# Kernel tuning notes

Hardware: AMD Instinct MI355X
Metric: run time of the kernel (lower is better)

Reference implementation:

```python
import jax, jax.numpy as jnp
import numpy as np

B, C, H, W = 8, 2048, 14, 14
NUM_CLASSES, WORD_DIM, INTER_DIM = 80, 300, 1024


def setup_inputs() -> dict:
    key = jax.random.key(0)
    ks = jax.random.split(key, 8)
    s = 0.02
    return {
        "image_features": jax.random.normal(ks[0], (B, C, H, W), jnp.float32),
        "word_features": jax.random.normal(ks[1], (NUM_CLASSES, WORD_DIM), jnp.float32),
        "W1": jax.random.normal(ks[2], (INTER_DIM, C), jnp.float32) * s,
        "W2": jax.random.normal(ks[3], (INTER_DIM, WORD_DIM), jnp.float32) * s,
        "W3": jax.random.normal(ks[4], (INTER_DIM, INTER_DIM), jnp.float32) * s,
        "b3": jax.random.normal(ks[5], (INTER_DIM,), jnp.float32) * s,
        "Wa": jax.random.normal(ks[6], (1, INTER_DIM), jnp.float32) * s,
        "ba": jax.random.normal(ks[7], (1,), jnp.float32) * s,
        "num_classes": NUM_CLASSES,
    }


def reference(image_features, word_features, W1, W2, W3, b3, Wa, ba, num_classes):
    b, c, h, w = image_features.shape
    # [s, b, c] with s = h*w (spatial locations)
    img = image_features.reshape(b, c, h * w).transpose(2, 0, 1)
    f_wh = img @ W1.T                      # [s, b, D]
    f_wd = word_features @ W2.T            # [n, D]
    # additive-attention score MLP; broadcast to [s, b, n, D]
    lb = jnp.tanh(f_wh[:, :, None, :] * f_wd[None, None, :, :]) @ W3.T + b3
    coef = (lb @ Wa.T + ba)[..., 0]        # [s, b, n]
    coef = jax.nn.softmax(coef, axis=0)    # softmax over spatial locations
    # weighted sum over spatial dim -> [b, n, c]
    return jnp.einsum('sbc,sbn->bnc', img, coef)
```

## Files before the change

kernel.cpp:

```cpp
#include <hip/hip_runtime.h>
#include <math.h>

#define SB 196
#define SP 224
#define NB 8
#define NC 2048
#define ND 1024
#define NN 80
#define NW 300
#define CH 8
#define DCH (ND / CH)

typedef __bf16 v8bf __attribute__((ext_vector_type(8)));
typedef __bf16 v4bf __attribute__((ext_vector_type(4)));
typedef __bf16 v2bf __attribute__((ext_vector_type(2)));
typedef float  f32x4 __attribute__((ext_vector_type(4)));

__global__ __launch_bounds__(256) void k0_v(const float* __restrict__ W3,
                                            const float* __restrict__ Wa,
                                            float* __restrict__ v) {
    int d  = blockIdx.x * 256 + threadIdx.x;
    int e0 = blockIdx.y * 64;
    float p = 0.f;
    #pragma unroll 8
    for (int e = e0; e < e0 + 64; ++e) {
        p += Wa[e] * W3[(size_t)e * ND + d];
    }
    atomicAdd(&v[d], p);
}

__global__ __launch_bounds__(256) void k0_fwd(const float* __restrict__ word,
                                              const float* __restrict__ W2,
                                              const float* __restrict__ v,
                                              float2* __restrict__ wpack) {
    __shared__ __align__(16) float lword[NW];
    int n = blockIdx.x;
    int d = blockIdx.y * 256 + threadIdx.x;
    for (int i = threadIdx.x; i < NW; i += 256) lword[i] = word[(size_t)n * NW + i];
    __syncthreads();
    const float4* wr = (const float4*)(W2 + (size_t)d * NW);
    const float4* l4 = (const float4*)lword;
    float acc = 0.f;
    #pragma unroll 5
    for (int i = 0; i < NW / 4; ++i) {
        float4 a = wr[i], b = l4[i];
        acc += a.x * b.x + a.y * b.y + a.z * b.z + a.w * b.w;
    }
    float2 o;
    o.x = 2.8853900817779268f * acc;
    o.y = -2.f * v[d];
    wpack[(size_t)n * ND + d] = o;
}

__global__ __launch_bounds__(256) void kcast_x(const float* __restrict__ X,
                                               const float* __restrict__ W1,
                                               __bf16* __restrict__ Xt,
                                               __bf16* __restrict__ Xhi,
                                               __bf16* __restrict__ Xlo,
                                               __bf16* __restrict__ W1b) {
    const int t = threadIdx.x;
    if (blockIdx.z == 8) {
        unsigned int slice_tid = (blockIdx.x * 4 + blockIdx.y) * 256 + t;
        #pragma unroll 4
        for (int r = 0; r < 16; ++r) {
            size_t i = ((size_t)slice_tid + (size_t)r * 32768) * 4;
            float4 f = *(const float4*)(W1 + i);
            v4bf o;
            o[0] = (__bf16)f.x; o[1] = (__bf16)f.y;
            o[2] = (__bf16)f.z; o[3] = (__bf16)f.w;
            *(v4bf*)(W1b + i) = o;
        }
        return;
    }
    __shared__ float tile[64][65];
    const int b  = blockIdx.z;
    const int c0 = blockIdx.x * 64;
    const int s0 = blockIdx.y * 64;
    const float* Xb = X + (size_t)b * NC * SB;
    {
        int ss = t & 63, cbase = t >> 6;
        #pragma unroll
        for (int r = 0; r < 16; ++r) {
            int cc = cbase + 4 * r;
            float val = (s0 + ss < SB) ? Xb[(size_t)(c0 + cc) * SB + s0 + ss] : 0.f;
            tile[cc][ss] = val;
        }
    }
    __syncthreads();
    {
        int cc = t & 63, sbase = t >> 6;
        #pragma unroll
        for (int r = 0; r < 16; ++r) {
            int ss = sbase + 4 * r;
            if (s0 + ss < SB)
                Xt[((size_t)b * SB + s0 + ss) * NC + c0 + cc] = (__bf16)tile[cc][ss];
        }
    }
    {
        int ss = t & 63, cbase = t >> 6;
        int sg = s0 + ss;
        #pragma unroll
        for (int r = 0; r < 16; ++r) {
            int cc = cbase + 4 * r;
            if (sg < SP) {
                float val = (sg < SB) ? tile[cc][ss] : 0.f;
                __bf16 h = (__bf16)val;
                __bf16 l = (__bf16)(val - (float)h);
                size_t base = ((size_t)b * NC + c0 + cc) * SP + sg;
                Xhi[base] = h;
                Xlo[base] = l;
            }
        }
    }
}

#define PITCH 40
__global__ __launch_bounds__(256) void k1_mfma(const __bf16* __restrict__ Xt,
                                               const __bf16* __restrict__ W1b,
                                               float* __restrict__ F) {
    __shared__ __align__(16) __bf16 lA[64 * PITCH];
    __shared__ __align__(16) __bf16 lB[64 * PITCH];
    const int t    = threadIdx.x;
    const int d0   = blockIdx.x * 64;
    const int s0   = blockIdx.y * 64;
    const int b    = blockIdx.z;
    const int lane = t & 63;
    const int wave = t >> 6;
    const int doff = (wave & 1) * 32;
    const int soff = (wave >> 1) * 32;
    const int quad = lane >> 4;
    const int l16  = lane & 15;

    f32x4 acc[2][2] = {};

    const int rr = t >> 2;
    const int cc = (t & 3) * 8;
    const bool sv = (s0 + rr) < SB;
    const __bf16* Ag = W1b + (size_t)(d0 + rr) * NC + cc;
    const __bf16* Bg = Xt + ((size_t)b * SB + (sv ? (s0 + rr) : 0)) * NC + cc;
    __bf16* lAw = lA + rr * PITCH + cc;
    __bf16* lBw = lB + rr * PITCH + cc;

    const __bf16* rA0 = lA + (doff + l16) * PITCH + quad * 8;
    const __bf16* rA1 = rA0 + 16 * PITCH;
    const __bf16* rB0 = lB + (soff + l16) * PITCH + quad * 8;
    const __bf16* rB1 = rB0 + 16 * PITCH;

    for (int k0 = 0; k0 < NC; k0 += 32) {
        uint4 a = *(const uint4*)(Ag + k0);
        uint4 bv = sv ? *(const uint4*)(Bg + k0) : make_uint4(0u, 0u, 0u, 0u);
        __syncthreads();
        *(uint4*)lAw = a;
        *(uint4*)lBw = bv;
        __syncthreads();
        v8bf a0 = *(const v8bf*)rA0;
        v8bf a1 = *(const v8bf*)rA1;
        v8bf b0 = *(const v8bf*)rB0;
        v8bf b1 = *(const v8bf*)rB1;
        acc[0][0] = __builtin_amdgcn_mfma_f32_16x16x32_bf16(a0, b0, acc[0][0], 0, 0, 0);
        acc[0][1] = __builtin_amdgcn_mfma_f32_16x16x32_bf16(a0, b1, acc[0][1], 0, 0, 0);
        acc[1][0] = __builtin_amdgcn_mfma_f32_16x16x32_bf16(a1, b0, acc[1][0], 0, 0, 0);
        acc[1][1] = __builtin_amdgcn_mfma_f32_16x16x32_bf16(a1, b1, acc[1][1], 0, 0, 0);
    }
    float* Fb = F + (size_t)b * ND * SB;
    #pragma unroll
    for (int i = 0; i < 2; ++i) {
        #pragma unroll
        for (int j = 0; j < 2; ++j) {
            int s = s0 + soff + j * 16 + l16;
            if (s < SB) {
                #pragma unroll
                for (int r = 0; r < 4; ++r) {
                    int d = d0 + doff + i * 16 + quad * 4 + r;
                    Fb[(size_t)d * SB + s] = acc[i][j][r];
                }
            }
        }
    }
}

__global__ __launch_bounds__(256) void k2a(const float* __restrict__ F,
                                           const float2* __restrict__ wpack,
                                           float* __restrict__ part) {
    const int n0  = blockIdx.x * 4;
    const int ch  = blockIdx.z;
    const int idx = blockIdx.y * 256 + threadIdx.x;
    const bool valid = idx < (NB * SB);
    const int iv = valid ? idx : 0;
    const int b  = iv / SB;
    const int s  = iv - b * SB;
    const float*  Fp  = F + ((size_t)b * ND + ch * DCH) * SB + s;
    const float4* wp0 = (const float4*)(wpack + (size_t)(n0 + 0) * ND + ch * DCH);
    const float4* wp1 = (const float4*)(wpack + (size_t)(n0 + 1) * ND + ch * DCH);
    const float4* wp2 = (const float4*)(wpack + (size_t)(n0 + 2) * ND + ch * DCH);
    const float4* wp3 = (const float4*)(wpack + (size_t)(n0 + 3) * ND + ch * DCH);
    float a0 = 0.f, a1 = 0.f, a2 = 0.f, a3 = 0.f;
    #pragma unroll 4
    for (int d2 = 0; d2 < DCH / 2; ++d2) {
        float f0 = Fp[(size_t)(2 * d2)     * SB];
        float f1 = Fp[(size_t)(2 * d2 + 1) * SB];
        float4 w0 = wp0[d2];
        float4 w1 = wp1[d2];
        float4 w2 = wp2[d2];
        float4 w3 = wp3[d2];
        float e00 = __builtin_amdgcn_exp2f(f0 * w0.x);
        float e01 = __builtin_amdgcn_exp2f(f1 * w0.z);
        float e10 = __builtin_amdgcn_exp2f(f0 * w1.x);
        float e11 = __builtin_amdgcn_exp2f(f1 * w1.z);
        float e20 = __builtin_amdgcn_exp2f(f0 * w2.x);
        float e21 = __builtin_amdgcn_exp2f(f1 * w2.z);
        float e30 = __builtin_amdgcn_exp2f(f0 * w3.x);
        float e31 = __builtin_amdgcn_exp2f(f1 * w3.z);
        a0 = fmaf(w0.y, __builtin_amdgcn_rcpf(1.f + e00), a0);
        a0 = fmaf(w0.w, __builtin_amdgcn_rcpf(1.f + e01), a0);
        a1 = fmaf(w1.y, __builtin_amdgcn_rcpf(1.f + e10), a1);
        a1 = fmaf(w1.w, __builtin_amdgcn_rcpf(1.f + e11), a1);
        a2 = fmaf(w2.y, __builtin_amdgcn_rcpf(1.f + e20), a2);
        a2 = fmaf(w2.w, __builtin_amdgcn_rcpf(1.f + e21), a2);
        a3 = fmaf(w3.y, __builtin_amdgcn_rcpf(1.f + e30), a3);
        a3 = fmaf(w3.w, __builtin_amdgcn_rcpf(1.f + e31), a3);
    }
    if (valid) {
        size_t base = ((size_t)ch * NB + b) * NN;
        part[(base + n0 + 0) * 256 + s] = a0;
        part[(base + n0 + 1) * 256 + s] = a1;
        part[(base + n0 + 2) * 256 + s] = a2;
        part[(base + n0 + 3) * 256 + s] = a3;
    }
}

__global__ __launch_bounds__(256) void k2b(const float* __restrict__ part,
                                           __bf16* __restrict__ coefh,
                                           __bf16* __restrict__ coefl) {
    __shared__ float red[256];
    const int n = blockIdx.x;
    const int b = blockIdx.y;
    const int t = threadIdx.x;
    float acc = 0.f;
    #pragma unroll
    for (int ch = 0; ch < CH; ++ch)
        acc += part[(((size_t)ch * NB + b) * NN + n) * 256 + t];

    red[t] = (t < SB) ? acc : -1e30f;
    __syncthreads();
    #pragma unroll
    for (int off = 128; off > 0; off >>= 1) {
        if (t < off) red[t] = fmaxf(red[t], red[t + off]);
        __syncthreads();
    }
    float m = red[0];
    __syncthreads();
    float p = (t < SB) ? __expf(acc - m) : 0.f;
    red[t] = p;
    __syncthreads();
    #pragma unroll
    for (int off = 128; off > 0; off >>= 1) {
        if (t < off) red[t] += red[t + off];
        __syncthreads();
    }
    float inv = 1.f / red[0];
    if (t < SP) {
        float val = (t < SB) ? p * inv : 0.f;
        __bf16 h = (__bf16)val;
        __bf16 l = (__bf16)(val - (float)h);
        size_t base = ((size_t)b * NN + n) * SP + t;
        coefh[base] = h;
        coefl[base] = l;
    }
}

__global__ __launch_bounds__(256) void k3_mfma(const __bf16* __restrict__ Xhi,
                                               const __bf16* __restrict__ Xlo,
                                               const __bf16* __restrict__ coefh,
                                               const __bf16* __restrict__ coefl,
                                               float* __restrict__ out) {
    const int t     = threadIdx.x;
    const int wave  = t >> 6;
    const int lane  = t & 63;
    const int quad  = lane >> 4;
    const int l16   = lane & 15;
    const int b     = blockIdx.y;
    const int cbase = blockIdx.x * 64 + wave * 16;

    const __bf16* Bh = Xhi + ((size_t)b * NC + cbase + l16) * SP + quad * 8;
    const __bf16* Bl = Xlo + ((size_t)b * NC + cbase + l16) * SP + quad * 8;
    const __bf16* Ah = coefh + ((size_t)b * NN + l16) * SP + quad * 8;
    const __bf16* Al = coefl + ((size_t)b * NN + l16) * SP + quad * 8;

    f32x4 acc[5] = {};

    #pragma unroll
    for (int k0 = 0; k0 < SP; k0 += 32) {
        v8bf bh = *(const v8bf*)(Bh + k0);
        v8bf bl = *(const v8bf*)(Bl + k0);
        #pragma unroll
        for (int mt = 0; mt < 5; ++mt) {
            v8bf ah = *(const v8bf*)(Ah + (size_t)mt * 16 * SP + k0);
            v8bf al = *(const v8bf*)(Al + (size_t)mt * 16 * SP + k0);
            acc[mt] = __builtin_amdgcn_mfma_f32_16x16x32_bf16(ah, bh, acc[mt], 0, 0, 0);
            acc[mt] = __builtin_amdgcn_mfma_f32_16x16x32_bf16(al, bh, acc[mt], 0, 0, 0);
            acc[mt] = __builtin_amdgcn_mfma_f32_16x16x32_bf16(ah, bl, acc[mt], 0, 0, 0);
        }
    }
    #pragma unroll
    for (int mt = 0; mt < 5; ++mt) {
        #pragma unroll
        for (int r = 0; r < 4; ++r) {
            int n = mt * 16 + quad * 4 + r;
            out[((size_t)b * NN + n) * NC + cbase + l16] = acc[mt][r];
        }
    }
}

extern "C" void kernel_launch(void* const* d_in, const int* in_sizes, int n_in,
                              void* d_out, int out_size, void* d_ws, size_t ws_size,
                              hipStream_t stream) {
    const float* X    = (const float*)d_in[0];
    const float* word = (const float*)d_in[1];
    const float* W1   = (const float*)d_in[2];
    const float* W2   = (const float*)d_in[3];
    const float* W3   = (const float*)d_in[4];
    const float* Wa   = (const float*)d_in[6];
    float* out = (float*)d_out;

    char* ws = (char*)d_ws;
    float*  v     = (float*)ws;
    float2* wpack = (float2*)(v + ND);
    float*  part  = (float*)(wpack + (size_t)NN * ND);
    __bf16* coefh = (__bf16*)(part + (size_t)CH * NB * NN * 256);
    __bf16* coefl = coefh + (size_t)NB * NN * SP;
    __bf16* W1b   = coefl + (size_t)NB * NN * SP;
    __bf16* Xt    = W1b + (size_t)ND * NC;
    float*  F     = (float*)(Xt + (size_t)NB * SB * NC);
    __bf16* Xhi   = (__bf16*)(F + (size_t)NB * ND * SB);
    __bf16* Xlo   = Xhi + (size_t)NB * NC * SP;

    hipMemsetAsync(v, 0, ND * sizeof(float), stream);
    k0_v   <<<dim3(4, 16),       256, 0, stream>>>(W3, Wa, v);
    k0_fwd <<<dim3(NN, 4),       256, 0, stream>>>(word, W2, v, wpack);
    kcast_x<<<dim3(32, 4, 9),    256, 0, stream>>>(X, W1, Xt, Xhi, Xlo, W1b);
    k1_mfma<<<dim3(16, 4, NB),   256, 0, stream>>>(Xt, W1b, F);
    k2a    <<<dim3(NN / 4, 7, CH), 256, 0, stream>>>(F, wpack, part);
    k2b    <<<dim3(NN, NB),      256, 0, stream>>>(part, coefh, coefl);
    k3_mfma<<<dim3(NC / 64, NB), 256, 0, stream>>>(Xhi, Xlo, coefh, coefl, out);
}
```

Measured before the change: 188.0 us.

## Fuse W1 projection GEMM with attention score reduction via LDS tile

Merges the bf16 MFMA projection kernel with the tanh-score partial reduction. Each block now stages its 64x64 F tile in shared memory and evaluates the per-class score sums directly, writing partials chunked by the 16 d-blocks (CH raised to 16). This removes the global round trip of the full F tensor and one launch. In exchange, the score work is limited to the 512 GEMM blocks with serial per-wave class loops, a 64-register array per thread, and twice as many partials for the reduction kernel to sum.

```diff
diff --git a/kernel.cpp b/kernel.cpp
--- a/kernel.cpp
+++ b/kernel.cpp
@@ -8,12 +8,10 @@
 #define ND 1024
 #define NN 80
 #define NW 300
-#define CH 8
-#define DCH (ND / CH)
+#define CH 16
 
 typedef __bf16 v8bf __attribute__((ext_vector_type(8)));
 typedef __bf16 v4bf __attribute__((ext_vector_type(4)));
-typedef __bf16 v2bf __attribute__((ext_vector_type(2)));
 typedef float  f32x4 __attribute__((ext_vector_type(4)));
 
 __global__ __launch_bounds__(256) void k0_v(const float* __restrict__ W3,
@@ -115,11 +113,14 @@
 }
 
 #define PITCH 40
-__global__ __launch_bounds__(256) void k1_mfma(const __bf16* __restrict__ Xt,
-                                               const __bf16* __restrict__ W1b,
-                                               float* __restrict__ F) {
+#define FP 66
+__global__ __launch_bounds__(256) void k12(const __bf16* __restrict__ Xt,
+                                           const __bf16* __restrict__ W1b,
+                                           const float2* __restrict__ wpack,
+                                           float* __restrict__ part) {
     __shared__ __align__(16) __bf16 lA[64 * PITCH];
     __shared__ __align__(16) __bf16 lB[64 * PITCH];
+    __shared__ __align__(16) float ldsF[64 * FP];
     const int t    = threadIdx.x;
     const int d0   = blockIdx.x * 64;
     const int s0   = blockIdx.y * 64;
@@ -162,70 +163,39 @@
         acc[1][0] = __builtin_amdgcn_mfma_f32_16x16x32_bf16(a1, b0, acc[1][0], 0, 0, 0);
         acc[1][1] = __builtin_amdgcn_mfma_f32_16x16x32_bf16(a1, b1, acc[1][1], 0, 0, 0);
     }
-    float* Fb = F + (size_t)b * ND * SB;
     #pragma unroll
     for (int i = 0; i < 2; ++i) {
         #pragma unroll
         for (int j = 0; j < 2; ++j) {
-            int s = s0 + soff + j * 16 + l16;
-            if (s < SB) {
-                #pragma unroll
-                for (int r = 0; r < 4; ++r) {
-                    int d = d0 + doff + i * 16 + quad * 4 + r;
-                    Fb[(size_t)d * SB + s] = acc[i][j][r];
-                }
+            int sl = soff + j * 16 + l16;
+            #pragma unroll
+            for (int r = 0; r < 4; ++r) {
+                int dl = doff + i * 16 + quad * 4 + r;
+                ldsF[dl * FP + sl] = acc[i][j][r];
             }
         }
     }
-}
-
-__global__ __launch_bounds__(256) void k2a(const float* __restrict__ F,
-                                           const float2* __restrict__ wpack,
-                                           float* __restrict__ part) {
-    const int n0  = blockIdx.x * 4;
-    const int ch  = blockIdx.z;
-    const int idx = blockIdx.y * 256 + threadIdx.x;
-    const bool valid = idx < (NB * SB);
-    const int iv = valid ? idx : 0;
-    const int b  = iv / SB;
-    const int s  = iv - b * SB;
-    const float*  Fp  = F + ((size_t)b * ND + ch * DCH) * SB + s;
-    const float4* wp0 = (const float4*)(wpack + (size_t)(n0 + 0) * ND + ch * DCH);
-    const float4* wp1 = (const float4*)(wpack + (size_t)(n0 + 1) * ND + ch * DCH);
-    const float4* wp2 = (const float4*)(wpack + (size_t)(n0 + 2) * ND + ch * DCH);
-    const float4* wp3 = (const float4*)(wpack + (size_t)(n0 + 3) * ND + ch * DCH);
-    float a0 = 0.f, a1 = 0.f, a2 = 0.f, a3 = 0.f;
-    #pragma unroll 4
-    for (int d2 = 0; d2 < DCH / 2; ++d2) {
-        float f0 = Fp[(size_t)(2 * d2)     * SB];
-        float f1 = Fp[(size_t)(2 * d2 + 1) * SB];
-        float4 w0 = wp0[d2];
-        float4 w1 = wp1[d2];
-        float4 w2 = wp2[d2];
-        float4 w3 = wp3[d2];
-        float e00 = __builtin_amdgcn_exp2f(f0 * w0.x);
-        float e01 = __builtin_amdgcn_exp2f(f1 * w0.z);
-        float e10 = __builtin_amdgcn_exp2f(f0 * w1.x);
-        float e11 = __builtin_amdgcn_exp2f(f1 * w1.z);
-        float e20 = __builtin_amdgcn_exp2f(f0 * w2.x);
-        float e21 = __builtin_amdgcn_exp2f(f1 * w2.z);
-        float e30 = __builtin_amdgcn_exp2f(f0 * w3.x);
-        float e31 = __builtin_amdgcn_exp2f(f1 * w3.z);
-        a0 = fmaf(w0.y, __builtin_amdgcn_rcpf(1.f + e00), a0);
-        a0 = fmaf(w0.w, __builtin_amdgcn_rcpf(1.f + e01), a0);
-        a1 = fmaf(w1.y, __builtin_amdgcn_rcpf(1.f + e10), a1);
-        a1 = fmaf(w1.w, __builtin_amdgcn_rcpf(1.f + e11), a1);
-        a2 = fmaf(w2.y, __builtin_amdgcn_rcpf(1.f + e20), a2);
-        a2 = fmaf(w2.w, __builtin_amdgcn_rcpf(1.f + e21), a2);
-        a3 = fmaf(w3.y, __builtin_amdgcn_rcpf(1.f + e30), a3);
-        a3 = fmaf(w3.w, __builtin_amdgcn_rcpf(1.f + e31), a3);
-    }
-    if (valid) {
-        size_t base = ((size_t)ch * NB + b) * NN;
-        part[(base + n0 + 0) * 256 + s] = a0;
-        part[(base + n0 + 1) * 256 + s] = a1;
-        part[(base + n0 + 2) * 256 + s] = a2;
-        part[(base + n0 + 3) * 256 + s] = a3;
+    __syncthreads();
+    float fv[64];
+    #pragma unroll
+    for (int d = 0; d < 64; ++d) fv[d] = ldsF[d * FP + lane];
+    const int sg = s0 + lane;
+    const bool svalid = sg < SB;
+    const int nbase = wave * 20;
+    float* pbase = part + (((size_t)blockIdx.x * NB + b) * NN) * 256;
+    for (int nn = 0; nn < 20; ++nn) {
+        int n = nbase + nn;
+        const float4* wp4 = (const float4*)(wpack + (size_t)n * ND + d0);
+        float a2 = 0.f;
+        #pragma unroll
+        for (int d2 = 0; d2 < 32; ++d2) {
+            float4 w = wp4[d2];
+            float e0 = __builtin_amdgcn_exp2f(fv[2 * d2]     * w.x);
+            float e1 = __builtin_amdgcn_exp2f(fv[2 * d2 + 1] * w.z);
+            a2 = fmaf(w.y, __builtin_amdgcn_rcpf(1.f + e0), a2);
+            a2 = fmaf(w.w, __builtin_amdgcn_rcpf(1.f + e1), a2);
+        }
+        if (svalid) pbase[(size_t)n * 256 + sg] = a2;
     }
 }
 
@@ -331,16 +301,14 @@
     __bf16* coefl = coefh + (size_t)NB * NN * SP;
     __bf16* W1b   = coefl + (size_t)NB * NN * SP;
     __bf16* Xt    = W1b + (size_t)ND * NC;
-    float*  F     = (float*)(Xt + (size_t)NB * SB * NC);
-    __bf16* Xhi   = (__bf16*)(F + (size_t)NB * ND * SB);
+    __bf16* Xhi   = Xt + (size_t)NB * SB * NC;
     __bf16* Xlo   = Xhi + (size_t)NB * NC * SP;
 
     hipMemsetAsync(v, 0, ND * sizeof(float), stream);
     k0_v   <<<dim3(4, 16),       256, 0, stream>>>(W3, Wa, v);
     k0_fwd <<<dim3(NN, 4),       256, 0, stream>>>(word, W2, v, wpack);
     kcast_x<<<dim3(32, 4, 9),    256, 0, stream>>>(X, W1, Xt, Xhi, Xlo, W1b);
-    k1_mfma<<<dim3(16, 4, NB),   256, 0, stream>>>(Xt, W1b, F);
-    k2a    <<<dim3(NN / 4, 7, CH), 256, 0, stream>>>(F, wpack, part);
+    k12    <<<dim3(16, 4, NB),   256, 0, stream>>>(Xt, W1b, wpack, part);
     k2b    <<<dim3(NN, NB),      256, 0, stream>>>(part, coefh, coefl);
     k3_mfma<<<dim3(NC / 64, NB), 256, 0, stream>>>(Xhi, Xlo, coefh, coefl, out);
 }
```

New measurement: 195.0 us. +3.7%, slower.
